# Kernel optimization log

Hardware: AMD Instinct MI355X
Metric: run time of the kernel (lower is better)

The kernel has to match this reference:

```python
import jax, jax.numpy as jnp
import numpy as np

N_HEADS = 16
D_EMBD = 1024
B, T = 2, 2048


def setup_inputs() -> dict:
    key = jax.random.key(0)
    k1, k2, k3 = jax.random.split(key, 3)
    x = jax.random.normal(k1, (B, T, D_EMBD), dtype=jnp.float32)
    W1 = jax.random.normal(k2, (D_EMBD, 3 * D_EMBD), dtype=jnp.float32) / np.sqrt(D_EMBD)
    b1 = jnp.zeros((3 * D_EMBD,), dtype=jnp.float32)
    W2 = jax.random.normal(k3, (D_EMBD, D_EMBD), dtype=jnp.float32) / np.sqrt(D_EMBD)
    b2 = jnp.zeros((D_EMBD,), dtype=jnp.float32)
    return {"x": x, "W1": W1, "b1": b1, "W2": W2, "b2": b2}


def reference(x, W1, b1, W2, b2):
    bs, t, d = x.shape
    h = N_HEADS
    kqv = x @ W1 + b1  # [b, t, 3d]
    # note original split order: k, q, v
    k, q, v = jnp.split(kqv, 3, axis=-1)
    # [b, t, d] -> [b, h, t, dh]
    def to_heads(z):
        return z.reshape(bs, t, h, d // h).transpose(0, 2, 1, 3)
    k, q, v = to_heads(k), to_heads(q), to_heads(v)
    mask = jnp.tril(jnp.ones((t, t), dtype=bool))
    attn = jnp.where(mask, jnp.einsum('bhqd,bhkd->bhqk', q, k), 0.0)  # softmax-free retention
    out = jnp.einsum('bhqk,bhkd->bhqd', attn, v)
    out = out.transpose(0, 2, 1, 3).reshape(bs, t, d)  # [b, t, d]
    return out @ W2 + b2
```

## Files before the change

### kernel.cpp

```cpp
#include <hip/hip_runtime.h>
#include <hip/hip_bf16.h>

typedef __bf16 bf16x8 __attribute__((ext_vector_type(8)));
typedef float f32x4 __attribute__((ext_vector_type(4)));
typedef float f32x16 __attribute__((ext_vector_type(16)));
typedef unsigned short ushort_t;
typedef unsigned short ushort8 __attribute__((ext_vector_type(8)));
typedef unsigned int uint4v __attribute__((ext_vector_type(4)));


__device__ inline void gload_lds16(const void* g, void* l) {
  __builtin_amdgcn_global_load_lds(
      (const __attribute__((address_space(1))) void*)g,
      (__attribute__((address_space(3))) void*)l, 16, 0, 0);
}

__device__ inline ushort_t f2bf(float f) {
  unsigned int u = __float_as_uint(f);
  unsigned int lsb = (u >> 16) & 1u;
  u += 0x7fffu + lsb;
  return (ushort_t)(u >> 16);
}


__device__ inline void transpose_tile_f32_bf16(
    const float* __restrict__ in, ushort_t* __restrict__ out,
    int R, int C, int cx, int ry, int tid) {
  __shared__ float tile[32][33];
  const int tx = tid & 31, ty = tid >> 5;
  const int c0 = cx * 32, r0 = ry * 32;
#pragma unroll
  for (int i = 0; i < 32; i += 8)
    tile[ty + i][tx] = in[(size_t)(r0 + ty + i) * C + c0 + tx];
  __syncthreads();
#pragma unroll
  for (int i = 0; i < 32; i += 8)
    out[(size_t)(c0 + ty + i) * R + r0 + tx] = f2bf(tile[tx][ty + i]);
}

__global__ __launch_bounds__(256) void prep_kernel(
    const float* __restrict__ x, const float* __restrict__ W1,
    const float* __restrict__ W2, ushort_t* __restrict__ xb,
    ushort_t* __restrict__ w1t, ushort_t* __restrict__ w2t) {
  const int bid = blockIdx.x;
  const int tid = threadIdx.x;
  if (bid < 2048) {
    int i = (bid * 256 + tid) * 8;
    float4 a = *(const float4*)&x[i];
    float4 b = *(const float4*)&x[i + 4];
    ushort8 o;
    o[0] = f2bf(a.x); o[1] = f2bf(a.y); o[2] = f2bf(a.z); o[3] = f2bf(a.w);
    o[4] = f2bf(b.x); o[5] = f2bf(b.y); o[6] = f2bf(b.z); o[7] = f2bf(b.w);
    *(ushort8*)&xb[i] = o;
  } else if (bid < 2048 + 3072) {
    const int t = bid - 2048;
    transpose_tile_f32_bf16(W1, w1t, 1024, 3072, t % 96, t / 96, tid);
  } else {
    const int t = bid - 5120;
    transpose_tile_f32_bf16(W2, w2t, 1024, 1024, t % 32, t / 32, tid);
  }
}

__global__ __launch_bounds__(256) void transpose_v(
    const ushort_t* __restrict__ kqv, ushort_t* __restrict__ vt) {
  __shared__ ushort_t tile[64 * 64];
  const int tt = blockIdx.x;
  const int bh = blockIdx.y;
  const int b = bh >> 4, h = bh & 15;
  const int tid = threadIdx.x;
#pragma unroll
  for (int p = 0; p < 2; p++) {
    const int tr = (tid >> 3) + p * 32;
    const int c8 = tid & 7;
    ushort8 v = *(const ushort8*)&kqv[(size_t)(b * 2048 + tt * 64 + tr) * 3072 +
                                      2048 + h * 64 + c8 * 8];
    *(ushort8*)&tile[tr * 64 + ((c8 ^ (tr & 7)) * 8)] = v;
  }
  __syncthreads();
  const int d = tid & 63;
#pragma unroll
  for (int p = 0; p < 2; p++) {
    const int t8 = (tid >> 6) + p * 4;
    ushort8 o;
#pragma unroll
    for (int j = 0; j < 8; j++) {
      const int t = t8 * 8 + j;
      o[j] = tile[t * 64 + (((d >> 3) ^ (t & 7)) * 8) + (d & 7)];
    }
    *(ushort8*)&vt[(size_t)(bh * 64 + d) * 2048 + tt * 64 + t8 * 8] = o;
  }
}


template <bool OUT_BF16>
__global__ __launch_bounds__(256) void gemm_bt(
    const ushort_t* __restrict__ A, const ushort_t* __restrict__ BT,
    const float* __restrict__ bias, void* __restrict__ Cout,
    int M, int N, int K) {
  __shared__ ushort_t lA[3][128 * 32];
  __shared__ ushort_t lB[3][128 * 32];
  const int tid = threadIdx.x;
  const int lane = tid & 63;
  const int wave = tid >> 6;
  const int wr = wave >> 1, wc = wave & 1;
  const int l16 = lane & 15, lhi = lane >> 4;
  const int bx = blockIdx.x, by = blockIdx.y;

  const int srow = tid >> 2;
  const int schunk = (tid & 3) ^ (srow & 3);
  const ushort_t* gA = A + (size_t)(by * 128 + srow) * K + schunk * 8;
  const ushort_t* gB = BT + (size_t)(bx * 128 + srow) * K + schunk * 8;

#define GSTAGE(buf, k0)                                            \
  do {                                                             \
    gload_lds16(gA + (k0), &lA[buf][tid * 8]);                     \
    gload_lds16(gA + (k0) + (size_t)64 * K, &lA[buf][tid * 8 + 2048]); \
    gload_lds16(gB + (k0), &lB[buf][tid * 8]);                     \
    gload_lds16(gB + (k0) + (size_t)64 * K, &lB[buf][tid * 8 + 2048]); \
  } while (0)

  f32x4 acc[4][4] = {};
  const int NK = K >> 5;

  GSTAGE(0, 0);
  GSTAGE(1, 32);

  int cur = 0;
  for (int kt = 0; kt < NK; ++kt) {
    if (kt + 1 < NK) asm volatile("s_waitcnt vmcnt(4)" ::: "memory");
    else             asm volatile("s_waitcnt vmcnt(0)" ::: "memory");
    __builtin_amdgcn_s_barrier();
    asm volatile("" ::: "memory");

    if (kt + 2 < NK) {
      const int pf = (cur + 2 >= 3) ? cur - 1 : cur + 2;
      GSTAGE(pf, (kt + 2) * 32);
    }

    bf16x8 af[4], bfr[4];
#pragma unroll
    for (int m = 0; m < 4; m++) {
      const int row = wr * 64 + m * 16 + l16;
      af[m] = *(const bf16x8*)&lA[cur][row * 32 + ((lhi ^ (row & 3)) * 8)];
    }
#pragma unroll
    for (int n = 0; n < 4; n++) {
      const int row = wc * 64 + n * 16 + l16;
      bfr[n] = *(const bf16x8*)&lB[cur][row * 32 + ((lhi ^ (row & 3)) * 8)];
    }
#pragma unroll
    for (int m = 0; m < 4; m++)
#pragma unroll
      for (int n = 0; n < 4; n++)
        acc[m][n] = __builtin_amdgcn_mfma_f32_16x16x32_bf16(af[m], bfr[n],
                                                            acc[m][n], 0, 0, 0);
    cur = (cur + 1 >= 3) ? 0 : cur + 1;
  }
#undef GSTAGE

  const int r0 = by * 128 + wr * 64 + lhi * 4;
  const int c0 = bx * 128 + wc * 64 + l16;
#pragma unroll
  for (int m = 0; m < 4; m++)
#pragma unroll
    for (int n = 0; n < 4; n++) {
      const int col = c0 + n * 16;
      const float bv = bias[col];
#pragma unroll
      for (int j = 0; j < 4; j++) {
        const int row = r0 + m * 16 + j;
        const float v = acc[m][n][j] + bv;
        if (OUT_BF16)
          ((ushort_t*)Cout)[(size_t)row * N + col] = f2bf(v);
        else
          ((float*)Cout)[(size_t)row * N + col] = v;
      }
    }
}


__global__ __launch_bounds__(256) void attn_kernel(
    const ushort_t* __restrict__ kqv, const ushort_t* __restrict__ vt,
    ushort_t* __restrict__ ao) {
  __shared__ ushort_t lK[2][64 * 64];
  __shared__ ushort_t lVT[2][64 * 64];
  const int tid = threadIdx.x, lane = tid & 63, wave = tid >> 6;
  const int q_rel = lane & 31, hi = lane >> 5;
  const int qs = wave & 1, kb = wave >> 1;
  const int L = blockIdx.x;
  const int xcd = L & 7, t = L >> 3;
  const int bh = xcd * 4 + (t >> 5);
  const int qj = 31 - ((t + bh * 7) & 31);
  const int b = bh >> 4, h = bh & 15;
  const ushort_t* base = kqv + (size_t)b * 2048 * 3072;
  const ushort_t* vbase = vt + (size_t)bh * 64 * 2048;

  size_t kg[2], vg[2];
  int ld[2];
#pragma unroll
  for (int p = 0; p < 2; p++) {
    const int slot = tid + p * 256;
    const int srow = slot >> 3;
    const int scb = (((slot & 7) * 16) ^ ((srow & 7) << 4)) >> 1;
    kg[p] = (size_t)srow * 3072 + h * 64 + scb;
    vg[p] = (size_t)srow * 2048 + scb;
    ld[p] = slot * 8;
  }

  const int wq0 = qj * 64 + qs * 32;
  bf16x8 qf[4];
#pragma unroll
  for (int ds = 0; ds < 4; ds++)
    qf[ds] = *(const bf16x8*)&base[(size_t)(wq0 + q_rel) * 3072 + 1024 + h * 64 +
                                   ds * 16 + hi * 8];

  f32x16 oacc[2] = {};
  const int nkt = qj + 1;

#pragma unroll
  for (int p = 0; p < 2; p++) {
    gload_lds16(&base[kg[p]], &lK[0][ld[p]]);
    gload_lds16(&vbase[vg[p]], &lVT[0][ld[p]]);
  }

  int cur = 0;
  for (int kt = 0; kt < nkt; ++kt) {
    asm volatile("s_waitcnt vmcnt(0)" ::: "memory");
    __builtin_amdgcn_s_barrier();
    asm volatile("" ::: "memory");

    if (kt + 1 < nkt) {
#pragma unroll
      for (int p = 0; p < 2; p++) {
        gload_lds16(&base[(size_t)(kt + 1) * 64 * 3072 + kg[p]], &lK[cur ^ 1][ld[p]]);
        gload_lds16(&vbase[(size_t)(kt + 1) * 64 + vg[p]], &lVT[cur ^ 1][ld[p]]);
      }
    }

    const int kv0 = kt * 64 + kb * 32;
    if (kv0 <= wq0 + 31) {
      f32x16 st = {};
      const int krow = kb * 32 + q_rel;
      const int ksw = krow & 7;
#pragma unroll
      for (int ds = 0; ds < 4; ds++) {
        bf16x8 kf = *(const bf16x8*)&lK[cur][krow * 64 + (((ds * 2 + hi) ^ ksw) * 8)];
        st = __builtin_amdgcn_mfma_f32_32x32x16_bf16(kf, qf[ds], st, 0, 0, 0);
      }
      if (kv0 + 31 > wq0) {
#pragma unroll
        for (int r = 0; r < 16; r++) {
          const int kgl = kv0 + (r & 3) + 8 * (r >> 2) + 4 * hi;
          if (kgl > wq0 + q_rel) st[r] = 0.f;
        }
      }
      unsigned int w0, w1, w2, w3, w4, w5, w6, w7;
      {
        float e0 = st[0], e1 = st[1], e2 = st[2], e3 = st[3];
        float e4 = st[4], e5 = st[5], e6 = st[6], e7 = st[7];
        float e8 = st[8], e9 = st[9], e10 = st[10], e11 = st[11];
        float e12 = st[12], e13 = st[13], e14 = st[14], e15 = st[15];
        asm("v_cvt_pk_bf16_f32 %0, %1, %2" : "=v"(w0) : "v"(e0), "v"(e1));
        asm("v_cvt_pk_bf16_f32 %0, %1, %2" : "=v"(w1) : "v"(e2), "v"(e3));
        asm("v_cvt_pk_bf16_f32 %0, %1, %2" : "=v"(w2) : "v"(e4), "v"(e5));
        asm("v_cvt_pk_bf16_f32 %0, %1, %2" : "=v"(w3) : "v"(e6), "v"(e7));
        asm("v_cvt_pk_bf16_f32 %0, %1, %2" : "=v"(w4) : "v"(e8), "v"(e9));
        asm("v_cvt_pk_bf16_f32 %0, %1, %2" : "=v"(w5) : "v"(e10), "v"(e11));
        asm("v_cvt_pk_bf16_f32 %0, %1, %2" : "=v"(w6) : "v"(e12), "v"(e13));
        asm("v_cvt_pk_bf16_f32 %0, %1, %2" : "=v"(w7) : "v"(e14), "v"(e15));
      }
      asm("v_permlane32_swap_b32 %0, %1" : "+v"(w0), "+v"(w2));
      asm("v_permlane32_swap_b32 %0, %1" : "+v"(w1), "+v"(w3));
      asm("v_permlane32_swap_b32 %0, %1" : "+v"(w4), "+v"(w6));
      asm("v_permlane32_swap_b32 %0, %1" : "+v"(w5), "+v"(w7));
      uint4v u0 = {w0, w1, w2, w3};
      uint4v u1 = {w4, w5, w6, w7};
      bf16x8 pa0 = __builtin_bit_cast(bf16x8, u0);
      bf16x8 pa1 = __builtin_bit_cast(bf16x8, u1);
#pragma unroll
      for (int dt = 0; dt < 2; dt++) {
        const int vrow = dt * 32 + q_rel;
        const int vsw = vrow & 7;
        bf16x8 vf0 = *(const bf16x8*)&lVT[cur][vrow * 64 + (((kb * 4 + hi) ^ vsw) * 8)];
        bf16x8 vf1 = *(const bf16x8*)&lVT[cur][vrow * 64 + (((kb * 4 + 2 + hi) ^ vsw) * 8)];
        oacc[dt] = __builtin_amdgcn_mfma_f32_32x32x16_bf16(pa0, vf0, oacc[dt], 0, 0, 0);
        oacc[dt] = __builtin_amdgcn_mfma_f32_32x32x16_bf16(pa1, vf1, oacc[dt], 0, 0, 0);
      }
    }

    cur ^= 1;
  }

  __syncthreads();
  float* red = (float*)&lK[0][0];
  if (kb == 1) {
#pragma unroll
    for (int dt = 0; dt < 2; dt++)
#pragma unroll
      for (int r = 0; r < 16; r++)
        red[qs * 2048 + (dt * 16 + r) * 64 + lane] = oacc[dt][r];
  }
  __syncthreads();
  if (kb == 0) {
#pragma unroll
    for (int dt = 0; dt < 2; dt++)
#pragma unroll
      for (int r = 0; r < 16; r++) {
        const float v = oacc[dt][r] + red[qs * 2048 + (dt * 16 + r) * 64 + lane];
        const int q = (r & 3) + 8 * (r >> 2) + 4 * hi;
        const int row = wq0 + q;
        const int col = h * 64 + dt * 32 + q_rel;
        ao[(size_t)(b * 2048 + row) * 1024 + col] = f2bf(v);
      }
  }
}


extern "C" void kernel_launch(void* const* d_in, const int* in_sizes, int n_in,
                              void* d_out, int out_size, void* d_ws, size_t ws_size,
                              hipStream_t stream) {
  const float* x  = (const float*)d_in[0];
  const float* W1 = (const float*)d_in[1];
  const float* b1 = (const float*)d_in[2];
  const float* W2 = (const float*)d_in[3];
  const float* b2 = (const float*)d_in[4];
  float* out = (float*)d_out;

  char* ws = (char*)d_ws;
  ushort_t* xb  = (ushort_t*)(ws);
  ushort_t* w1t = (ushort_t*)(ws + 8388608);
  ushort_t* w2t = (ushort_t*)(ws + 14680064);
  ushort_t* kqv = (ushort_t*)(ws + 16777216);
  ushort_t* ao  = (ushort_t*)(ws + 41943040);
  ushort_t* vtb = (ushort_t*)(ws);

  prep_kernel<<<6144, 256, 0, stream>>>(x, W1, W2, xb, w1t, w2t);
  gemm_bt<true ><<<dim3(24, 32), 256, 0, stream>>>(xb, w1t, b1, kqv, 4096, 3072, 1024);
  transpose_v<<<dim3(32, 32), 256, 0, stream>>>(kqv, vtb);
  attn_kernel<<<dim3(1024), 256, 0, stream>>>(kqv, vtb, ao);
  gemm_bt<false><<<dim3(8, 32), 256, 0, stream>>>(ao, w2t, b2, out, 4096, 1024, 1024);
}
```

Before: 187.0 us.

## Give each attention wave its own query rows with triple-buffered KV prefetch

The attention kernel now assigns 128 query rows per block (32 per wave) instead of 64, so each wave walks every key sub-tile itself. This removes the LDS cross-wave reduction and halves the grid to 512 blocks. K/V tiles are triple-buffered with a two-tile-ahead prefetch and a partial vmcnt wait, MFMA sections get raised priority, and the block-to-tile mapping pairs light and heavy causal tiles. The trade-off is more LDS per block, fewer blocks to spread across CUs, and longer per-wave serial work.

```diff
diff --git a/kernel.cpp b/kernel.cpp
--- a/kernel.cpp
+++ b/kernel.cpp
@@ -182,15 +182,15 @@
 __global__ __launch_bounds__(256) void attn_kernel(
     const ushort_t* __restrict__ kqv, const ushort_t* __restrict__ vt,
     ushort_t* __restrict__ ao) {
-  __shared__ ushort_t lK[2][64 * 64];
-  __shared__ ushort_t lVT[2][64 * 64];
+  __shared__ ushort_t lK[3][64 * 64];
+  __shared__ ushort_t lVT[3][64 * 64];
   const int tid = threadIdx.x, lane = tid & 63, wave = tid >> 6;
   const int q_rel = lane & 31, hi = lane >> 5;
-  const int qs = wave & 1, kb = wave >> 1;
   const int L = blockIdx.x;
-  const int xcd = L & 7, t = L >> 3;
-  const int bh = xcd * 4 + (t >> 5);
-  const int qj = 31 - ((t + bh * 7) & 31);
+  const int bh = L & 31;
+  const int k8 = (L >> 5) & 7;
+  const int qh = k8 * 2 + (bh & 1);
+  const int qj = (L < 256) ? qh : (15 - qh);
   const int b = bh >> 4, h = bh & 15;
   const ushort_t* base = kqv + (size_t)b * 2048 * 3072;
   const ushort_t* vbase = vt + (size_t)bh * 64 * 2048;
@@ -207,7 +207,7 @@
     ld[p] = slot * 8;
   }
 
-  const int wq0 = qj * 64 + qs * 32;
+  const int wq0 = qj * 128 + wave * 32;
   bf16x8 qf[4];
 #pragma unroll
   for (int ds = 0; ds < 4; ds++)
@@ -215,104 +215,105 @@
                                    ds * 16 + hi * 8];
 
   f32x16 oacc[2] = {};
-  const int nkt = qj + 1;
+  const int nkt = qj * 2 + 2;
 
 #pragma unroll
   for (int p = 0; p < 2; p++) {
     gload_lds16(&base[kg[p]], &lK[0][ld[p]]);
     gload_lds16(&vbase[vg[p]], &lVT[0][ld[p]]);
   }
+#pragma unroll
+  for (int p = 0; p < 2; p++) {
+    gload_lds16(&base[(size_t)64 * 3072 + kg[p]], &lK[1][ld[p]]);
+    gload_lds16(&vbase[64 + vg[p]], &lVT[1][ld[p]]);
+  }
 
   int cur = 0;
   for (int kt = 0; kt < nkt; ++kt) {
-    asm volatile("s_waitcnt vmcnt(0)" ::: "memory");
+    if (kt + 1 < nkt) asm volatile("s_waitcnt vmcnt(4)" ::: "memory");
+    else              asm volatile("s_waitcnt vmcnt(0)" ::: "memory");
     __builtin_amdgcn_s_barrier();
     asm volatile("" ::: "memory");
 
-    if (kt + 1 < nkt) {
+    if (kt + 2 < nkt) {
+      const int pf = (cur + 2 >= 3) ? cur - 1 : cur + 2;
 #pragma unroll
       for (int p = 0; p < 2; p++) {
-        gload_lds16(&base[(size_t)(kt + 1) * 64 * 3072 + kg[p]], &lK[cur ^ 1][ld[p]]);
-        gload_lds16(&vbase[(size_t)(kt + 1) * 64 + vg[p]], &lVT[cur ^ 1][ld[p]]);
+        gload_lds16(&base[(size_t)(kt + 2) * 64 * 3072 + kg[p]], &lK[pf][ld[p]]);
+        gload_lds16(&vbase[(size_t)(kt + 2) * 64 + vg[p]], &lVT[pf][ld[p]]);
       }
     }
 
-    const int kv0 = kt * 64 + kb * 32;
-    if (kv0 <= wq0 + 31) {
-      f32x16 st = {};
-      const int krow = kb * 32 + q_rel;
-      const int ksw = krow & 7;
-#pragma unroll
-      for (int ds = 0; ds < 4; ds++) {
-        bf16x8 kf = *(const bf16x8*)&lK[cur][krow * 64 + (((ds * 2 + hi) ^ ksw) * 8)];
-        st = __builtin_amdgcn_mfma_f32_32x32x16_bf16(kf, qf[ds], st, 0, 0, 0);
-      }
-      if (kv0 + 31 > wq0) {
-#pragma unroll
-        for (int r = 0; r < 16; r++) {
-          const int kgl = kv0 + (r & 3) + 8 * (r >> 2) + 4 * hi;
-          if (kgl > wq0 + q_rel) st[r] = 0.f;
+    if (kt * 64 <= wq0 + 31) {
+      __builtin_amdgcn_s_setprio(1);
+#pragma unroll
+      for (int kb = 0; kb < 2; kb++) {
+        const int kv0 = kt * 64 + kb * 32;
+        if (kv0 <= wq0 + 31) {
+          f32x16 st = {};
+          const int krow = kb * 32 + q_rel;
+          const int ksw = krow & 7;
+#pragma unroll
+          for (int ds = 0; ds < 4; ds++) {
+            bf16x8 kf = *(const bf16x8*)&lK[cur][krow * 64 + (((ds * 2 + hi) ^ ksw) * 8)];
+            st = __builtin_amdgcn_mfma_f32_32x32x16_bf16(kf, qf[ds], st, 0, 0, 0);
+          }
+          if (kv0 + 31 > wq0) {
+#pragma unroll
+            for (int r = 0; r < 16; r++) {
+              const int kgl = kv0 + (r & 3) + 8 * (r >> 2) + 4 * hi;
+              if (kgl > wq0 + q_rel) st[r] = 0.f;
+            }
+          }
+          unsigned int w0, w1, w2, w3, w4, w5, w6, w7;
+          {
+            float e0 = st[0], e1 = st[1], e2 = st[2], e3 = st[3];
+            float e4 = st[4], e5 = st[5], e6 = st[6], e7 = st[7];
+            float e8 = st[8], e9 = st[9], e10 = st[10], e11 = st[11];
+            float e12 = st[12], e13 = st[13], e14 = st[14], e15 = st[15];
+            asm("v_cvt_pk_bf16_f32 %0, %1, %2" : "=v"(w0) : "v"(e0), "v"(e1));
+            asm("v_cvt_pk_bf16_f32 %0, %1, %2" : "=v"(w1) : "v"(e2), "v"(e3));
+            asm("v_cvt_pk_bf16_f32 %0, %1, %2" : "=v"(w2) : "v"(e4), "v"(e5));
+            asm("v_cvt_pk_bf16_f32 %0, %1, %2" : "=v"(w3) : "v"(e6), "v"(e7));
+            asm("v_cvt_pk_bf16_f32 %0, %1, %2" : "=v"(w4) : "v"(e8), "v"(e9));
+            asm("v_cvt_pk_bf16_f32 %0, %1, %2" : "=v"(w5) : "v"(e10), "v"(e11));
+            asm("v_cvt_pk_bf16_f32 %0, %1, %2" : "=v"(w6) : "v"(e12), "v"(e13));
+            asm("v_cvt_pk_bf16_f32 %0, %1, %2" : "=v"(w7) : "v"(e14), "v"(e15));
+          }
+          asm("v_permlane32_swap_b32 %0, %1" : "+v"(w0), "+v"(w2));
+          asm("v_permlane32_swap_b32 %0, %1" : "+v"(w1), "+v"(w3));
+          asm("v_permlane32_swap_b32 %0, %1" : "+v"(w4), "+v"(w6));
+          asm("v_permlane32_swap_b32 %0, %1" : "+v"(w5), "+v"(w7));
+          uint4v u0 = {w0, w1, w2, w3};
+          uint4v u1 = {w4, w5, w6, w7};
+          bf16x8 pa0 = __builtin_bit_cast(bf16x8, u0);
+          bf16x8 pa1 = __builtin_bit_cast(bf16x8, u1);
+#pragma unroll
+          for (int dt = 0; dt < 2; dt++) {
+            const int vrow = dt * 32 + q_rel;
+            const int vsw = vrow & 7;
+            bf16x8 vf0 = *(const bf16x8*)&lVT[cur][vrow * 64 + (((kb * 4 + hi) ^ vsw) * 8)];
+            bf16x8 vf1 = *(const bf16x8*)&lVT[cur][vrow * 64 + (((kb * 4 + 2 + hi) ^ vsw) * 8)];
+            oacc[dt] = __builtin_amdgcn_mfma_f32_32x32x16_bf16(pa0, vf0, oacc[dt], 0, 0, 0);
+            oacc[dt] = __builtin_amdgcn_mfma_f32_32x32x16_bf16(pa1, vf1, oacc[dt], 0, 0, 0);
+          }
         }
       }
-      unsigned int w0, w1, w2, w3, w4, w5, w6, w7;
-      {
-        float e0 = st[0], e1 = st[1], e2 = st[2], e3 = st[3];
-        float e4 = st[4], e5 = st[5], e6 = st[6], e7 = st[7];
-        float e8 = st[8], e9 = st[9], e10 = st[10], e11 = st[11];
-        float e12 = st[12], e13 = st[13], e14 = st[14], e15 = st[15];
-        asm("v_cvt_pk_bf16_f32 %0, %1, %2" : "=v"(w0) : "v"(e0), "v"(e1));
-        asm("v_cvt_pk_bf16_f32 %0, %1, %2" : "=v"(w1) : "v"(e2), "v"(e3));
-        asm("v_cvt_pk_bf16_f32 %0, %1, %2" : "=v"(w2) : "v"(e4), "v"(e5));
-        asm("v_cvt_pk_bf16_f32 %0, %1, %2" : "=v"(w3) : "v"(e6), "v"(e7));
-        asm("v_cvt_pk_bf16_f32 %0, %1, %2" : "=v"(w4) : "v"(e8), "v"(e9));
-        asm("v_cvt_pk_bf16_f32 %0, %1, %2" : "=v"(w5) : "v"(e10), "v"(e11));
-        asm("v_cvt_pk_bf16_f32 %0, %1, %2" : "=v"(w6) : "v"(e12), "v"(e13));
-        asm("v_cvt_pk_bf16_f32 %0, %1, %2" : "=v"(w7) : "v"(e14), "v"(e15));
-      }
-      asm("v_permlane32_swap_b32 %0, %1" : "+v"(w0), "+v"(w2));
-      asm("v_permlane32_swap_b32 %0, %1" : "+v"(w1), "+v"(w3));
-      asm("v_permlane32_swap_b32 %0, %1" : "+v"(w4), "+v"(w6));
-      asm("v_permlane32_swap_b32 %0, %1" : "+v"(w5), "+v"(w7));
-      uint4v u0 = {w0, w1, w2, w3};
-      uint4v u1 = {w4, w5, w6, w7};
-      bf16x8 pa0 = __builtin_bit_cast(bf16x8, u0);
-      bf16x8 pa1 = __builtin_bit_cast(bf16x8, u1);
-#pragma unroll
-      for (int dt = 0; dt < 2; dt++) {
-        const int vrow = dt * 32 + q_rel;
-        const int vsw = vrow & 7;
-        bf16x8 vf0 = *(const bf16x8*)&lVT[cur][vrow * 64 + (((kb * 4 + hi) ^ vsw) * 8)];
-        bf16x8 vf1 = *(const bf16x8*)&lVT[cur][vrow * 64 + (((kb * 4 + 2 + hi) ^ vsw) * 8)];
-        oacc[dt] = __builtin_amdgcn_mfma_f32_32x32x16_bf16(pa0, vf0, oacc[dt], 0, 0, 0);
-        oacc[dt] = __builtin_amdgcn_mfma_f32_32x32x16_bf16(pa1, vf1, oacc[dt], 0, 0, 0);
-      }
-    }
-
-    cur ^= 1;
-  }
-
-  __syncthreads();
-  float* red = (float*)&lK[0][0];
-  if (kb == 1) {
-#pragma unroll
-    for (int dt = 0; dt < 2; dt++)
-#pragma unroll
-      for (int r = 0; r < 16; r++)
-        red[qs * 2048 + (dt * 16 + r) * 64 + lane] = oacc[dt][r];
-  }
-  __syncthreads();
-  if (kb == 0) {
-#pragma unroll
-    for (int dt = 0; dt < 2; dt++)
-#pragma unroll
-      for (int r = 0; r < 16; r++) {
-        const float v = oacc[dt][r] + red[qs * 2048 + (dt * 16 + r) * 64 + lane];
-        const int q = (r & 3) + 8 * (r >> 2) + 4 * hi;
-        const int row = wq0 + q;
-        const int col = h * 64 + dt * 32 + q_rel;
-        ao[(size_t)(b * 2048 + row) * 1024 + col] = f2bf(v);
-      }
-  }
+      __builtin_amdgcn_s_setprio(0);
+    }
+
+    cur = (cur + 1 >= 3) ? 0 : cur + 1;
+  }
+
+#pragma unroll
+  for (int dt = 0; dt < 2; dt++)
+#pragma unroll
+    for (int r = 0; r < 16; r++) {
+      const int q = (r & 3) + 8 * (r >> 2) + 4 * hi;
+      const int row = wq0 + q;
+      const int col = h * 64 + dt * 32 + q_rel;
+      ao[(size_t)(b * 2048 + row) * 1024 + col] = f2bf(oacc[dt][r]);
+    }
 }
 
 
@@ -337,6 +338,6 @@
   prep_kernel<<<6144, 256, 0, stream>>>(x, W1, W2, xb, w1t, w2t);
   gemm_bt<true ><<<dim3(24, 32), 256, 0, stream>>>(xb, w1t, b1, kqv, 4096, 3072, 1024);
   transpose_v<<<dim3(32, 32), 256, 0, stream>>>(kqv, vtb);
-  attn_kernel<<<dim3(1024), 256, 0, stream>>>(kqv, vtb, ao);
+  attn_kernel<<<dim3(512), 256, 0, stream>>>(kqv, vtb, ao);
   gemm_bt<false><<<dim3(8, 32), 256, 0, stream>>>(ao, w2t, b2, out, 4096, 1024, 1024);
 }
```

Result: slower. 194.7 us (+4.2%).

## Make attention kernel persistent with atomic work queue, longest tiles first

Applied to the files above, without the earlier changes.

Switches the causal attention kernel from one block per (head, query-tile) to a persistent grid of 512 blocks that pull work items from a global atomic counter. Items are ordered so the longest query tiles (most key tiles) are dispatched first, which balances the triangular workload across CUs. The cost is an extra memset launch, one atomic plus two barriers per item, and the loss of the previous XCD-aware block-to-head mapping that favoured L2 locality.

```diff
diff --git a/kernel.cpp b/kernel.cpp
--- a/kernel.cpp
+++ b/kernel.cpp
@@ -181,137 +181,146 @@
 
 __global__ __launch_bounds__(256) void attn_kernel(
     const ushort_t* __restrict__ kqv, const ushort_t* __restrict__ vt,
-    ushort_t* __restrict__ ao) {
+    ushort_t* __restrict__ ao, int* __restrict__ counter) {
   __shared__ ushort_t lK[2][64 * 64];
   __shared__ ushort_t lVT[2][64 * 64];
+  __shared__ int s_item;
   const int tid = threadIdx.x, lane = tid & 63, wave = tid >> 6;
   const int q_rel = lane & 31, hi = lane >> 5;
   const int qs = wave & 1, kb = wave >> 1;
-  const int L = blockIdx.x;
-  const int xcd = L & 7, t = L >> 3;
-  const int bh = xcd * 4 + (t >> 5);
-  const int qj = 31 - ((t + bh * 7) & 31);
-  const int b = bh >> 4, h = bh & 15;
-  const ushort_t* base = kqv + (size_t)b * 2048 * 3072;
-  const ushort_t* vbase = vt + (size_t)bh * 64 * 2048;
-
-  size_t kg[2], vg[2];
+
+  size_t kgo[2], vgo[2];
   int ld[2];
 #pragma unroll
   for (int p = 0; p < 2; p++) {
     const int slot = tid + p * 256;
     const int srow = slot >> 3;
     const int scb = (((slot & 7) * 16) ^ ((srow & 7) << 4)) >> 1;
-    kg[p] = (size_t)srow * 3072 + h * 64 + scb;
-    vg[p] = (size_t)srow * 2048 + scb;
+    kgo[p] = (size_t)srow * 3072 + scb;
+    vgo[p] = (size_t)srow * 2048 + scb;
     ld[p] = slot * 8;
   }
 
-  const int wq0 = qj * 64 + qs * 32;
-  bf16x8 qf[4];
-#pragma unroll
-  for (int ds = 0; ds < 4; ds++)
-    qf[ds] = *(const bf16x8*)&base[(size_t)(wq0 + q_rel) * 3072 + 1024 + h * 64 +
-                                   ds * 16 + hi * 8];
-
-  f32x16 oacc[2] = {};
-  const int nkt = qj + 1;
-
-#pragma unroll
-  for (int p = 0; p < 2; p++) {
-    gload_lds16(&base[kg[p]], &lK[0][ld[p]]);
-    gload_lds16(&vbase[vg[p]], &lVT[0][ld[p]]);
-  }
-
-  int cur = 0;
-  for (int kt = 0; kt < nkt; ++kt) {
-    asm volatile("s_waitcnt vmcnt(0)" ::: "memory");
-    __builtin_amdgcn_s_barrier();
-    asm volatile("" ::: "memory");
-
-    if (kt + 1 < nkt) {
-#pragma unroll
-      for (int p = 0; p < 2; p++) {
-        gload_lds16(&base[(size_t)(kt + 1) * 64 * 3072 + kg[p]], &lK[cur ^ 1][ld[p]]);
-        gload_lds16(&vbase[(size_t)(kt + 1) * 64 + vg[p]], &lVT[cur ^ 1][ld[p]]);
+  for (;;) {
+    __syncthreads();
+    if (tid == 0) s_item = atomicAdd(counter, 1);
+    __syncthreads();
+    const int w = s_item;
+    if (w >= 1024) break;
+
+    const int qj = 31 - (w >> 5);
+    const int bh = w & 31;
+    const int b = bh >> 4, h = bh & 15;
+    const ushort_t* base = kqv + (size_t)b * 2048 * 3072;
+    const ushort_t* vbase = vt + (size_t)bh * 64 * 2048;
+    const size_t kg0 = kgo[0] + h * 64, kg1 = kgo[1] + h * 64;
+
+    const int wq0 = qj * 64 + qs * 32;
+    bf16x8 qf[4];
+#pragma unroll
+    for (int ds = 0; ds < 4; ds++)
+      qf[ds] = *(const bf16x8*)&base[(size_t)(wq0 + q_rel) * 3072 + 1024 + h * 64 +
+                                     ds * 16 + hi * 8];
+
+    f32x16 oacc[2] = {};
+    const int nkt = qj + 1;
+
+    gload_lds16(&base[kg0], &lK[0][ld[0]]);
+    gload_lds16(&base[kg1], &lK[0][ld[1]]);
+    gload_lds16(&vbase[vgo[0]], &lVT[0][ld[0]]);
+    gload_lds16(&vbase[vgo[1]], &lVT[0][ld[1]]);
+
+    int cur = 0;
+    for (int kt = 0; kt < nkt; ++kt) {
+      asm volatile("s_waitcnt vmcnt(0)" ::: "memory");
+      __builtin_amdgcn_s_barrier();
+      asm volatile("" ::: "memory");
+
+      if (kt + 1 < nkt) {
+        const size_t koff = (size_t)(kt + 1) * 64 * 3072;
+        const size_t voff = (size_t)(kt + 1) * 64;
+        gload_lds16(&base[koff + kg0], &lK[cur ^ 1][ld[0]]);
+        gload_lds16(&base[koff + kg1], &lK[cur ^ 1][ld[1]]);
+        gload_lds16(&vbase[voff + vgo[0]], &lVT[cur ^ 1][ld[0]]);
+        gload_lds16(&vbase[voff + vgo[1]], &lVT[cur ^ 1][ld[1]]);
       }
-    }
-
-    const int kv0 = kt * 64 + kb * 32;
-    if (kv0 <= wq0 + 31) {
-      f32x16 st = {};
-      const int krow = kb * 32 + q_rel;
-      const int ksw = krow & 7;
-#pragma unroll
-      for (int ds = 0; ds < 4; ds++) {
-        bf16x8 kf = *(const bf16x8*)&lK[cur][krow * 64 + (((ds * 2 + hi) ^ ksw) * 8)];
-        st = __builtin_amdgcn_mfma_f32_32x32x16_bf16(kf, qf[ds], st, 0, 0, 0);
+
+      const int kv0 = kt * 64 + kb * 32;
+      if (kv0 <= wq0 + 31) {
+        f32x16 st = {};
+        const int krow = kb * 32 + q_rel;
+        const int ksw = krow & 7;
+#pragma unroll
+        for (int ds = 0; ds < 4; ds++) {
+          bf16x8 kf = *(const bf16x8*)&lK[cur][krow * 64 + (((ds * 2 + hi) ^ ksw) * 8)];
+          st = __builtin_amdgcn_mfma_f32_32x32x16_bf16(kf, qf[ds], st, 0, 0, 0);
+        }
+        if (kv0 + 31 > wq0) {
+#pragma unroll
+          for (int r = 0; r < 16; r++) {
+            const int kgl = kv0 + (r & 3) + 8 * (r >> 2) + 4 * hi;
+            if (kgl > wq0 + q_rel) st[r] = 0.f;
+          }
+        }
+        unsigned int w0, w1, w2, w3, w4, w5, w6, w7;
+        {
+          float e0 = st[0], e1 = st[1], e2 = st[2], e3 = st[3];
+          float e4 = st[4], e5 = st[5], e6 = st[6], e7 = st[7];
+          float e8 = st[8], e9 = st[9], e10 = st[10], e11 = st[11];
+          float e12 = st[12], e13 = st[13], e14 = st[14], e15 = st[15];
+          asm("v_cvt_pk_bf16_f32 %0, %1, %2" : "=v"(w0) : "v"(e0), "v"(e1));
+          asm("v_cvt_pk_bf16_f32 %0, %1, %2" : "=v"(w1) : "v"(e2), "v"(e3));
+          asm("v_cvt_pk_bf16_f32 %0, %1, %2" : "=v"(w2) : "v"(e4), "v"(e5));
+          asm("v_cvt_pk_bf16_f32 %0, %1, %2" : "=v"(w3) : "v"(e6), "v"(e7));
+          asm("v_cvt_pk_bf16_f32 %0, %1, %2" : "=v"(w4) : "v"(e8), "v"(e9));
+          asm("v_cvt_pk_bf16_f32 %0, %1, %2" : "=v"(w5) : "v"(e10), "v"(e11));
+          asm("v_cvt_pk_bf16_f32 %0, %1, %2" : "=v"(w6) : "v"(e12), "v"(e13));
+          asm("v_cvt_pk_bf16_f32 %0, %1, %2" : "=v"(w7) : "v"(e14), "v"(e15));
+        }
+        asm("v_permlane32_swap_b32 %0, %1" : "+v"(w0), "+v"(w2));
+        asm("v_permlane32_swap_b32 %0, %1" : "+v"(w1), "+v"(w3));
+        asm("v_permlane32_swap_b32 %0, %1" : "+v"(w4), "+v"(w6));
+        asm("v_permlane32_swap_b32 %0, %1" : "+v"(w5), "+v"(w7));
+        uint4v u0 = {w0, w1, w2, w3};
+        uint4v u1 = {w4, w5, w6, w7};
+        bf16x8 pa0 = __builtin_bit_cast(bf16x8, u0);
+        bf16x8 pa1 = __builtin_bit_cast(bf16x8, u1);
+#pragma unroll
+        for (int dt = 0; dt < 2; dt++) {
+          const int vrow = dt * 32 + q_rel;
+          const int vsw = vrow & 7;
+          bf16x8 vf0 = *(const bf16x8*)&lVT[cur][vrow * 64 + (((kb * 4 + hi) ^ vsw) * 8)];
+          bf16x8 vf1 = *(const bf16x8*)&lVT[cur][vrow * 64 + (((kb * 4 + 2 + hi) ^ vsw) * 8)];
+          oacc[dt] = __builtin_amdgcn_mfma_f32_32x32x16_bf16(pa0, vf0, oacc[dt], 0, 0, 0);
+          oacc[dt] = __builtin_amdgcn_mfma_f32_32x32x16_bf16(pa1, vf1, oacc[dt], 0, 0, 0);
+        }
       }
-      if (kv0 + 31 > wq0) {
+
+      cur ^= 1;
+    }
+
+    __syncthreads();
+    float* red = (float*)&lK[0][0];
+    if (kb == 1) {
+#pragma unroll
+      for (int dt = 0; dt < 2; dt++)
+#pragma unroll
+        for (int r = 0; r < 16; r++)
+          red[qs * 2048 + (dt * 16 + r) * 64 + lane] = oacc[dt][r];
+    }
+    __syncthreads();
+    if (kb == 0) {
+#pragma unroll
+      for (int dt = 0; dt < 2; dt++)
 #pragma unroll
         for (int r = 0; r < 16; r++) {
-          const int kgl = kv0 + (r & 3) + 8 * (r >> 2) + 4 * hi;
-          if (kgl > wq0 + q_rel) st[r] = 0.f;
-        }
-      }
-      unsigned int w0, w1, w2, w3, w4, w5, w6, w7;
-      {
-        float e0 = st[0], e1 = st[1], e2 = st[2], e3 = st[3];
-        float e4 = st[4], e5 = st[5], e6 = st[6], e7 = st[7];
-        float e8 = st[8], e9 = st[9], e10 = st[10], e11 = st[11];
-        float e12 = st[12], e13 = st[13], e14 = st[14], e15 = st[15];
-        asm("v_cvt_pk_bf16_f32 %0, %1, %2" : "=v"(w0) : "v"(e0), "v"(e1));
-        asm("v_cvt_pk_bf16_f32 %0, %1, %2" : "=v"(w1) : "v"(e2), "v"(e3));
-        asm("v_cvt_pk_bf16_f32 %0, %1, %2" : "=v"(w2) : "v"(e4), "v"(e5));
-        asm("v_cvt_pk_bf16_f32 %0, %1, %2" : "=v"(w3) : "v"(e6), "v"(e7));
-        asm("v_cvt_pk_bf16_f32 %0, %1, %2" : "=v"(w4) : "v"(e8), "v"(e9));
-        asm("v_cvt_pk_bf16_f32 %0, %1, %2" : "=v"(w5) : "v"(e10), "v"(e11));
-        asm("v_cvt_pk_bf16_f32 %0, %1, %2" : "=v"(w6) : "v"(e12), "v"(e13));
-        asm("v_cvt_pk_bf16_f32 %0, %1, %2" : "=v"(w7) : "v"(e14), "v"(e15));
-      }
-      asm("v_permlane32_swap_b32 %0, %1" : "+v"(w0), "+v"(w2));
-      asm("v_permlane32_swap_b32 %0, %1" : "+v"(w1), "+v"(w3));
-      asm("v_permlane32_swap_b32 %0, %1" : "+v"(w4), "+v"(w6));
-      asm("v_permlane32_swap_b32 %0, %1" : "+v"(w5), "+v"(w7));
-      uint4v u0 = {w0, w1, w2, w3};
-      uint4v u1 = {w4, w5, w6, w7};
-      bf16x8 pa0 = __builtin_bit_cast(bf16x8, u0);
-      bf16x8 pa1 = __builtin_bit_cast(bf16x8, u1);
-#pragma unroll
-      for (int dt = 0; dt < 2; dt++) {
-        const int vrow = dt * 32 + q_rel;
-        const int vsw = vrow & 7;
-        bf16x8 vf0 = *(const bf16x8*)&lVT[cur][vrow * 64 + (((kb * 4 + hi) ^ vsw) * 8)];
-        bf16x8 vf1 = *(const bf16x8*)&lVT[cur][vrow * 64 + (((kb * 4 + 2 + hi) ^ vsw) * 8)];
-        oacc[dt] = __builtin_amdgcn_mfma_f32_32x32x16_bf16(pa0, vf0, oacc[dt], 0, 0, 0);
-        oacc[dt] = __builtin_amdgcn_mfma_f32_32x32x16_bf16(pa1, vf1, oacc[dt], 0, 0, 0);
-      }
-    }
-
-    cur ^= 1;
-  }
-
-  __syncthreads();
-  float* red = (float*)&lK[0][0];
-  if (kb == 1) {
-#pragma unroll
-    for (int dt = 0; dt < 2; dt++)
-#pragma unroll
-      for (int r = 0; r < 16; r++)
-        red[qs * 2048 + (dt * 16 + r) * 64 + lane] = oacc[dt][r];
-  }
-  __syncthreads();
-  if (kb == 0) {
-#pragma unroll
-    for (int dt = 0; dt < 2; dt++)
-#pragma unroll
-      for (int r = 0; r < 16; r++) {
-        const float v = oacc[dt][r] + red[qs * 2048 + (dt * 16 + r) * 64 + lane];
-        const int q = (r & 3) + 8 * (r >> 2) + 4 * hi;
-        const int row = wq0 + q;
-        const int col = h * 64 + dt * 32 + q_rel;
-        ao[(size_t)(b * 2048 + row) * 1024 + col] = f2bf(v);
-      }
+          const float v = oacc[dt][r] + red[qs * 2048 + (dt * 16 + r) * 64 + lane];
+          const int q = (r & 3) + 8 * (r >> 2) + 4 * hi;
+          const int row = wq0 + q;
+          const int col = h * 64 + dt * 32 + q_rel;
+          ao[(size_t)(b * 2048 + row) * 1024 + col] = f2bf(v);
+        }
+    }
   }
 }
 
@@ -333,10 +342,12 @@
   ushort_t* kqv = (ushort_t*)(ws + 16777216);
   ushort_t* ao  = (ushort_t*)(ws + 41943040);
   ushort_t* vtb = (ushort_t*)(ws);
-
+  int* counter  = (int*)(ws + 67108864);
+
+  hipMemsetAsync(counter, 0, 4, stream);
   prep_kernel<<<6144, 256, 0, stream>>>(x, W1, W2, xb, w1t, w2t);
   gemm_bt<true ><<<dim3(24, 32), 256, 0, stream>>>(xb, w1t, b1, kqv, 4096, 3072, 1024);
   transpose_v<<<dim3(32, 32), 256, 0, stream>>>(kqv, vtb);
-  attn_kernel<<<dim3(1024), 256, 0, stream>>>(kqv, vtb, ao);
+  attn_kernel<<<dim3(512), 256, 0, stream>>>(kqv, vtb, ao, counter);
   gemm_bt<false><<<dim3(8, 32), 256, 0, stream>>>(ao, w2t, b2, out, 4096, 1024, 1024);
 }
```

New measurement: 197.8 us. +5.8%, slower.
